# Kernel optimization log

Hardware: AMD Instinct MI355X
Metric: run time of the kernel (lower is better)

Reference implementation:

```python
import jax, jax.numpy as jnp
import numpy as np

B, T, D, K = 16, 4096, 512, 128
ALPHA_MIN = 1e-06
OMEGA_MAX = float(np.pi)
SN_EPS = 1e-06


def setup_inputs() -> dict:
    key = jax.random.key(0)
    ks = jax.random.split(key, 7)
    x = jax.random.normal(ks[0], (B, T, D), jnp.float32)
    # irregular positive step sizes, mean ~ 1/T like the uniform-grid default
    dt = jax.random.uniform(ks[1], (B, T), jnp.float32, minval=0.1, maxval=1.9) * (1.0 / T)
    # replicate reset_parameters: target_alpha ~ U(0.01, 0.2), raw = log(expm1(alpha - alpha_min))
    target_alpha = jax.random.uniform(ks[2], (K,), jnp.float32, minval=0.01, maxval=0.2)
    s_real_raw = jnp.log(jnp.expm1(jnp.maximum(target_alpha - ALPHA_MIN, 1e-08)))
    s_imag = jax.random.uniform(ks[3], (K,), jnp.float32, minval=-np.pi, maxval=np.pi)
    # kaiming-uniform-ish proj weight [K, D] and bias [K]
    W = jax.random.normal(ks[4], (K, D), jnp.float32) * (1.0 / np.sqrt(D))
    bound = 1.0 / np.sqrt(D)
    bias = jax.random.uniform(ks[5], (K,), jnp.float32, minval=-bound, maxval=bound)
    b_log = jnp.zeros((K,), jnp.float32)  # torch stores [1,1,K]; broadcasting is identical
    u_sn = jax.random.normal(ks[6], (K,), jnp.float32)  # spectral-norm power-iteration vector
    return {"x": x, "dt": dt, "s_real_raw": s_real_raw, "s_imag": s_imag,
            "W": W, "bias": bias, "b_log": b_log, "u_sn": u_sn}


def _spectral_normalize(W, u):
    # one power iteration, u/v detached (as torch.nn.utils.spectral_norm does)
    v = W.T @ u
    v = v / (jnp.linalg.norm(v) + SN_EPS)
    u2 = W @ v
    u2 = u2 / (jnp.linalg.norm(u2) + SN_EPS)
    u2 = jax.lax.stop_gradient(u2)
    v = jax.lax.stop_gradient(v)
    sigma = u2 @ (W @ v)
    return W / sigma


def reference(x, dt, s_real_raw, s_imag, W, bias, b_log, u_sn):
    # x: [B,T,D], dt: [B,T] -> lap_feats [B,T,2K]
    alpha = jax.nn.softplus(s_real_raw) + ALPHA_MIN          # [K] strictly positive decay
    omega = jnp.clip(s_imag, -OMEGA_MAX, OMEGA_MAX)          # [K]
    Wsn = _spectral_normalize(W, u_sn)
    u = jnp.einsum('btd,kd->btk', x, Wsn) + bias             # spectral-norm projection
    dt3 = dt[..., None]                                      # [B,T,1]
    rho = jnp.exp(-alpha * dt3)                              # [B,T,K]
    theta = omega * dt3
    cos_t, sin_t = jnp.cos(theta), jnp.sin(theta)
    b_gain = jnp.exp(b_log)                                  # [K]
    inj = (1.0 - rho) * (b_gain * u)                         # [B,T,K]

    def step(carry, inp):
        c, s = carry
        r, ct, st, it = inp
        c_new = r * (c * ct - s * st) + it
        s_new = r * (c * st + s * ct) + it
        return (c_new, s_new), (c_new, s_new)

    seq = (jnp.moveaxis(rho, 1, 0), jnp.moveaxis(cos_t, 1, 0),
           jnp.moveaxis(sin_t, 1, 0), jnp.moveaxis(inj, 1, 0))  # each [T,B,K]
    init = (jnp.zeros((x.shape[0], K), x.dtype), jnp.zeros((x.shape[0], K), x.dtype))
    _, (C, S) = jax.lax.scan(step, init, seq)
    C = jnp.moveaxis(C, 0, 1)  # [B,T,K]
    S = jnp.moveaxis(S, 0, 1)
    return jnp.concatenate([C, S], axis=-1)
```

## Files before the change

kernel.cpp:

```cpp
#include <hip/hip_runtime.h>
#include <stdint.h>

#define BB 16
#define TT 4096
#define DDIM 512
#define KK 128
#define TCB 128
#define NCB (TT / TCB)
#define PI_F 3.14159265358979323846f

typedef unsigned short u16;
typedef __attribute__((ext_vector_type(8))) short short8;
typedef __attribute__((ext_vector_type(4))) float f32x4;

__device__ __forceinline__ uint32_t cvt_bf16_rn(float f) {
  uint32_t u = __float_as_uint(f);
  return (u + 0x7FFFu + ((u >> 16) & 1u)) >> 16;
}
__device__ __forceinline__ uint32_t pack2(float a, float b) {
  return cvt_bf16_rn(a) | (cvt_bf16_rn(b) << 16);
}
__device__ __forceinline__ uint4 pack8(const float4 f0, const float4 f1) {
  uint4 r;
  r.x = pack2(f0.x, f0.y);
  r.y = pack2(f0.z, f0.w);
  r.z = pack2(f1.x, f1.y);
  r.w = pack2(f1.z, f1.w);
  return r;
}
__device__ __forceinline__ void gload_lds16(const void* g, void* l) {
  __builtin_amdgcn_global_load_lds(
      (const __attribute__((address_space(1))) void*)g,
      (__attribute__((address_space(3))) void*)l, 16, 0, 0);
}

__global__ __launch_bounds__(256) void k_prep(
    const float* __restrict__ W, const float* __restrict__ u_sn,
    const float* __restrict__ s_real_raw, const float* __restrict__ s_imag,
    const float* __restrict__ bias, const float* __restrict__ b_log,
    const float* __restrict__ dt,
    float* __restrict__ params, u16* __restrict__ Wp, float* __restrict__ ct) {
  int gb = blockIdx.x;
  int tid = threadIdx.x;
  if (gb < 64) {
    int idx = gb * 256 + tid;
    int k = idx >> 7;
    int d = (idx & 127) * 4;
    float4 v = *(const float4*)&W[(size_t)k * DDIM + d];
    int tile = d >> 6, dl = d & 63;
    int slot = (dl >> 3) ^ (k & 7);
    int e = dl & 7;
    size_t base = (size_t)tile * 8192 + k * 64 + slot * 8 + e;
    uint2 p;
    p.x = pack2(v.x, v.y);
    p.y = pack2(v.z, v.w);
    *(uint2*)&Wp[base] = p;
  } else if (gb < 80) {
    __shared__ float sc[256];
    int b = gb - 64;
    const float* row = dt + (size_t)b * TT;
    float* orow = ct + (size_t)b * TT;
    float loc[16];
    float s = 0.f;
    int base = tid * 16;
    for (int i = 0; i < 16; ++i) { s += row[base + i]; loc[i] = s; }
    sc[tid] = s;
    __syncthreads();
    for (int off = 1; off < 256; off <<= 1) {
      float v = (tid >= off) ? sc[tid - off] : 0.f;
      __syncthreads();
      sc[tid] += v;
      __syncthreads();
    }
    float excl = sc[tid] - s;
    for (int i = 0; i < 16; ++i) orow[base + i] = excl + loc[i];
  } else {
    __shared__ float su[KK];
    __shared__ float sv[DDIM];
    __shared__ float red[4];
    __shared__ float wred[256];
    __shared__ float s_sig;
    if (tid < KK) su[tid] = u_sn[tid];
    __syncthreads();
    for (int rep = 0; rep < 2; ++rep) {
      int d = tid + rep * 256;
      float acc = 0.f;
      for (int k = 0; k < KK; ++k) acc += W[k * DDIM + d] * su[k];
      sv[d] = acc;
    }
    __syncthreads();
    float nn = 0.f;
    for (int rep = 0; rep < 2; ++rep) { float v = sv[tid + rep * 256]; nn += v * v; }
    for (int off = 32; off > 0; off >>= 1) nn += __shfl_down(nn, off, 64);
    if ((tid & 63) == 0) red[tid >> 6] = nn;
    __syncthreads();
    float vn2 = red[0] + red[1] + red[2] + red[3];
    __syncthreads();
    float vinv = 1.f / (sqrtf(vn2) + 1e-6f);
    for (int rep = 0; rep < 2; ++rep) sv[tid + rep * 256] *= vinv;
    __syncthreads();
    {
      int k = tid & 127, q = tid >> 7;
      const float* wrow = W + (size_t)k * DDIM + q * 256;
      float p = 0.f;
      for (int d = 0; d < 256; ++d) p += wrow[d] * sv[q * 256 + d];
      wred[tid] = p;
    }
    __syncthreads();
    float wv = 0.f;
    if (tid < KK) wv = wred[tid] + wred[tid + 128];
    float q = wv * wv;
    for (int off = 32; off > 0; off >>= 1) q += __shfl_down(q, off, 64);
    if ((tid & 63) == 0) red[tid >> 6] = q;
    __syncthreads();
    if (tid == 0) {
      float wn2 = red[0] + red[1] + red[2] + red[3];
      s_sig = wn2 / (sqrtf(wn2) + 1e-6f);
    }
    __syncthreads();
    if (tid < KK) {
      float inv_sigma = 1.f / s_sig;
      float sr = s_real_raw[tid];
      float alpha = ((sr > 20.f) ? sr : log1pf(expf(sr))) + 1e-6f;
      float om = fminf(fmaxf(s_imag[tid], -PI_F), PI_F);
      float bg = expf(b_log[tid]);
      params[tid] = alpha;
      params[KK + tid] = om;
      params[2 * KK + tid] = bg * inv_sigma;
      params[3 * KK + tid] = bg * bias[tid];
    }
  }
}

__global__ __launch_bounds__(512, 4) void k_gemm(
    const float* __restrict__ x, const u16* __restrict__ Wp,
    const float* __restrict__ dt, const float* __restrict__ ct,
    const float* __restrict__ params, u16* __restrict__ itvb,
    float* __restrict__ csum_re, float* __restrict__ csum_im) {
  __shared__ __align__(16) u16 smem[32768];

  const int chunk = blockIdx.x, b = blockIdx.y;
  const int tid = threadIdx.x;
  const int wv = tid >> 6, l = tid & 63;
  const int lm = l & 15, lg = l >> 4;
  const int kw = wv & 1, tw = wv >> 1;
  const int t0 = chunk * TCB;

  const int xr = tid >> 2, xq = (tid & 3) * 16;
  const size_t xbase = ((size_t)b * TT + t0 + xr) * DDIM + xq;
  const int xs0 = ((xq >> 3) ^ (xr & 7)) * 8;
  const int xs1 = (((xq >> 3) + 1) ^ (xr & 7)) * 8;

  f32x4 acc[2][4];
#pragma unroll
  for (int m = 0; m < 2; ++m)
#pragma unroll
    for (int n = 0; n < 4; ++n) acc[m][n] = (f32x4)(0.0f);

  {
    const char* wsg = (const char*)Wp + (size_t)tid * 16;
    char* wd = (char*)smem + 32768 + tid * 16;
    gload_lds16(wsg, wd);
    gload_lds16(wsg + 8192, wd + 8192);
    const float* xp = x + xbase;
    float4 f0 = *(const float4*)(xp + 0);
    float4 f1 = *(const float4*)(xp + 4);
    float4 f2 = *(const float4*)(xp + 8);
    float4 f3 = *(const float4*)(xp + 12);
    *(uint4*)&smem[xr * 64 + xs0] = pack8(f0, f1);
    *(uint4*)&smem[xr * 64 + xs1] = pack8(f2, f3);
  }
  __syncthreads();

  int cur = 0;
  for (int it = 0; it < 8; ++it) {
    float4 f0, f1, f2, f3;
    if (it < 7) {
      const float* xp = x + xbase + (it + 1) * 64;
      f0 = *(const float4*)(xp + 0);
      f1 = *(const float4*)(xp + 4);
      f2 = *(const float4*)(xp + 8);
      f3 = *(const float4*)(xp + 12);
      const char* wsg = (const char*)Wp + (size_t)(it + 1) * 16384 + tid * 16;
      char* wd = (char*)smem + 32768 + (cur ^ 1) * 16384 + tid * 16;
      gload_lds16(wsg, wd);
      gload_lds16(wsg + 8192, wd + 8192);
    }
    __builtin_amdgcn_sched_barrier(0);
    {
      const u16* xb = smem + cur * 8192;
      const u16* wb = smem + 16384 + cur * 8192;
#pragma unroll
      for (int ks = 0; ks < 2; ++ks) {
        short8 fa[2], fb[4];
#pragma unroll
        for (int m = 0; m < 2; ++m) {
          int row = tw * 32 + m * 16 + lm;
          int sw = ((ks * 4 + lg) ^ (row & 7)) * 8;
          fa[m] = *(const short8*)&xb[row * 64 + sw];
        }
#pragma unroll
        for (int n = 0; n < 4; ++n) {
          int row = kw * 64 + n * 16 + lm;
          int sw = ((ks * 4 + lg) ^ (row & 7)) * 8;
          fb[n] = *(const short8*)&wb[row * 64 + sw];
        }
#pragma unroll
        for (int m = 0; m < 2; ++m)
#pragma unroll
          for (int n = 0; n < 4; ++n)
            acc[m][n] = __builtin_amdgcn_mfma_f32_16x16x32_bf16(fa[m], fb[n], acc[m][n], 0, 0, 0);
      }
    }
    __builtin_amdgcn_sched_barrier(0);
    if (it < 7) {
      u16* xb = smem + (cur ^ 1) * 8192;
      *(uint4*)&xb[xr * 64 + xs0] = pack8(f0, f1);
      *(uint4*)&xb[xr * 64 + xs1] = pack8(f2, f3);
    }
    __syncthreads();
    cur ^= 1;
  }

  float* totr = (float*)smem;
  float* toti = (float*)smem + 512;
  u16* litv = smem + 8192;

  float dtv[2][4], ctv[2][4];
#pragma unroll
  for (int m = 0; m < 2; ++m)
#pragma unroll
    for (int r = 0; r < 4; ++r) {
      int t = t0 + tw * 32 + m * 16 + lg * 4 + r;
      dtv[m][r] = dt[(size_t)b * TT + t];
      ctv[m][r] = ct[(size_t)b * TT + t];
    }

#pragma unroll
  for (int n = 0; n < 4; ++n) {
    int k = kw * 64 + n * 16 + lm;
    float pal = params[k], pom = params[KK + k];
    float pc1 = params[2 * KK + k], pc2 = params[3 * KK + k];
    float sr = 0.f, si2 = 0.f;
#pragma unroll
    for (int m = 0; m < 2; ++m)
#pragma unroll
      for (int r = 0; r < 4; ++r) {
        float g = acc[m][n][r];
        float a = pal * dtv[m][r];
        float omr = a * (1.f - a * (0.5f - a * (1.f / 6.f)));
        float itv = omr * (pc1 * g + pc2);
        int tl = tw * 32 + m * 16 + lg * 4 + r;
        litv[tl * KK + k] = (u16)cvt_bf16_rn(itv);
        float e = __expf(pal * ctv[m][r]);
        float sn, cs;
        __sincosf(pom * ctv[m][r], &sn, &cs);
        sr += itv * e * cs;
        si2 -= itv * e * sn;
      }
    sr += __shfl_xor(sr, 16, 64);
    sr += __shfl_xor(sr, 32, 64);
    si2 += __shfl_xor(si2, 16, 64);
    si2 += __shfl_xor(si2, 32, 64);
    if (lg == 0) { totr[tw * KK + k] = sr; toti[tw * KK + k] = si2; }
  }
  __syncthreads();

  if (tid < 256) {
    int v = tid & 127;
    float* src = (tid < 128) ? totr : toti;
    float* dst = (tid < 128) ? csum_re : csum_im;
    dst[((size_t)b * NCB + chunk) * KK + v] =
        (src[v] + src[KK + v]) + (src[2 * KK + v] + src[3 * KK + v]);
  }
  {
    int row = tid >> 4;
    int c8 = (tid & 15) * 8;
#pragma unroll
    for (int rr = 0; rr < 4; ++rr) {
      int tr = rr * 32 + row;
      uint4 v = *(const uint4*)&litv[tr * KK + c8];
      *(uint4*)&itvb[((size_t)b * TT + t0 + tr) * KK + c8] = v;
    }
  }
}

__global__ __launch_bounds__(512) void k_final(
    const u16* __restrict__ itvb, const float* __restrict__ ct,
    const float* __restrict__ params,
    const float* __restrict__ csum_re, const float* __restrict__ csum_im,
    float* __restrict__ out) {
  __shared__ float prer[KK], prei[KK];
  __shared__ float segr[16][KK], segi[16][KK];
  const int chunk = blockIdx.x, b = blockIdx.y;
  const int tid = threadIdx.x;
  const int k4 = (tid & 31) * 4, tseg = tid >> 5;
  const int tbase = chunk * TCB + tseg * 8;

  if (tid < 256) {
    int v = tid & 127;
    const float* srcp = (tid < 128) ? csum_re : csum_im;
    float* dstp = (tid < 128) ? prer : prei;
    size_t base = (size_t)b * NCB * KK + v;
    float a0 = 0.f, a1 = 0.f, a2 = 0.f, a3 = 0.f;
    int c = 0;
    for (; c + 4 <= chunk; c += 4) {
      a0 += srcp[base + (size_t)(c + 0) * KK];
      a1 += srcp[base + (size_t)(c + 1) * KK];
      a2 += srcp[base + (size_t)(c + 2) * KK];
      a3 += srcp[base + (size_t)(c + 3) * KK];
    }
    for (; c < chunk; ++c) a0 += srcp[base + (size_t)c * KK];
    dstp[v] = (a0 + a1) + (a2 + a3);
  }

  float4 pal4 = *(const float4*)&params[k4];
  float4 pom4 = *(const float4*)&params[KK + k4];
  float pal[4] = {pal4.x, pal4.y, pal4.z, pal4.w};
  float pom[4] = {pom4.x, pom4.y, pom4.z, pom4.w};

  uint2 iv8[8];
  float fr[8][4], fi[8][4];
  float sr[4] = {0.f, 0.f, 0.f, 0.f}, si[4] = {0.f, 0.f, 0.f, 0.f};
#pragma unroll
  for (int i = 0; i < 8; ++i) {
    int t = tbase + i;
    float ctv = ct[(size_t)b * TT + t];
    iv8[i] = *(const uint2*)&itvb[((size_t)b * TT + t) * KK + k4];
    float it[4] = {__uint_as_float(iv8[i].x << 16), __uint_as_float(iv8[i].x & 0xFFFF0000u),
                   __uint_as_float(iv8[i].y << 16), __uint_as_float(iv8[i].y & 0xFFFF0000u)};
#pragma unroll
    for (int c = 0; c < 4; ++c) {
      float e = __expf(pal[c] * ctv);
      float sn, cs;
      __sincosf(pom[c] * ctv, &sn, &cs);
      fr[i][c] = e * cs;
      fi[i][c] = e * sn;
      sr[c] += it[c] * fr[i][c];
      si[c] -= it[c] * fi[i][c];
    }
  }
  *(float4*)&segr[tseg][k4] = make_float4(sr[0], sr[1], sr[2], sr[3]);
  *(float4*)&segi[tseg][k4] = make_float4(si[0], si[1], si[2], si[3]);
  __syncthreads();
  float cr[4], ci[4];
  {
    float4 p0 = *(const float4*)&prer[k4];
    float4 p1 = *(const float4*)&prei[k4];
    cr[0] = p0.x; cr[1] = p0.y; cr[2] = p0.z; cr[3] = p0.w;
    ci[0] = p1.x; ci[1] = p1.y; ci[2] = p1.z; ci[3] = p1.w;
  }
  for (int s = 0; s < tseg; ++s) {
    float4 a = *(const float4*)&segr[s][k4];
    float4 bb = *(const float4*)&segi[s][k4];
    cr[0] += a.x; cr[1] += a.y; cr[2] += a.z; cr[3] += a.w;
    ci[0] += bb.x; ci[1] += bb.y; ci[2] += bb.z; ci[3] += bb.w;
  }
#pragma unroll
  for (int i = 0; i < 8; ++i) {
    int t = tbase + i;
    float it[4] = {__uint_as_float(iv8[i].x << 16), __uint_as_float(iv8[i].x & 0xFFFF0000u),
                   __uint_as_float(iv8[i].y << 16), __uint_as_float(iv8[i].y & 0xFFFF0000u)};
    float C4[4], S4[4];
#pragma unroll
    for (int c = 0; c < 4; ++c) {
      float f_r = fr[i][c], f_i = fi[i][c];
      cr[c] += it[c] * f_r;
      ci[c] -= it[c] * f_i;
      float inv = __builtin_amdgcn_rcpf(f_r * f_r + f_i * f_i);
      float Rw = (cr[c] * f_r - ci[c] * f_i) * inv;
      float Iw = (cr[c] * f_i + ci[c] * f_r) * inv;
      C4[c] = Rw - Iw;
      S4[c] = Rw + Iw;
    }
    size_t rowb = ((size_t)b * TT + t) * (2 * KK);
    *(float4*)&out[rowb + k4] = make_float4(C4[0], C4[1], C4[2], C4[3]);
    *(float4*)&out[rowb + KK + k4] = make_float4(S4[0], S4[1], S4[2], S4[3]);
  }
}

extern "C" void kernel_launch(void* const* d_in, const int* in_sizes, int n_in,
                              void* d_out, int out_size, void* d_ws, size_t ws_size,
                              hipStream_t stream) {
  const float* x    = (const float*)d_in[0];
  const float* dt   = (const float*)d_in[1];
  const float* srr  = (const float*)d_in[2];
  const float* si   = (const float*)d_in[3];
  const float* W    = (const float*)d_in[4];
  const float* bias = (const float*)d_in[5];
  const float* blog = (const float*)d_in[6];
  const float* usn  = (const float*)d_in[7];
  float* out = (float*)d_out;
  float* ws = (float*)d_ws;

  float* params  = ws;
  float* ct      = ws + 4 * KK;
  float* csum_re = ct + (size_t)BB * TT;
  float* csum_im = csum_re + (size_t)BB * NCB * KK;
  u16*   Wp      = (u16*)(csum_im + (size_t)BB * NCB * KK);
  u16*   itvb    = Wp + 65536;

  k_prep<<<81, 256, 0, stream>>>(W, usn, srr, si, bias, blog, dt, params, Wp, ct);
  k_gemm<<<dim3(NCB, BB), 512, 0, stream>>>(x, Wp, dt, ct, params, itvb,
                                            csum_re, csum_im);
  k_final<<<dim3(NCB, BB), 512, 0, stream>>>(itvb, ct, params,
                                             csum_re, csum_im, out);
}
```

Before: 67.52 us.

## Load GEMM operands directly from global into MFMA registers, drop LDS staging

The weight matrix is now prepacked in MFMA fragment order, so each lane loads its B fragment with one 16-byte global load. The x rows are read straight from global memory into registers and converted to bf16 in place. This removes the LDS double-buffer, the swizzled stores and the per-iteration barriers, and shrinks shared memory so more blocks can be resident. In exchange, x loads become strided per lane, W fragments are reread from L2 by every block, and there is less explicit prefetching.

```diff
diff --git a/kernel.cpp b/kernel.cpp
--- a/kernel.cpp
+++ b/kernel.cpp
@@ -20,18 +20,13 @@
 __device__ __forceinline__ uint32_t pack2(float a, float b) {
   return cvt_bf16_rn(a) | (cvt_bf16_rn(b) << 16);
 }
-__device__ __forceinline__ uint4 pack8(const float4 f0, const float4 f1) {
-  uint4 r;
-  r.x = pack2(f0.x, f0.y);
-  r.y = pack2(f0.z, f0.w);
-  r.z = pack2(f1.x, f1.y);
-  r.w = pack2(f1.z, f1.w);
-  return r;
-}
-__device__ __forceinline__ void gload_lds16(const void* g, void* l) {
-  __builtin_amdgcn_global_load_lds(
-      (const __attribute__((address_space(1))) void*)g,
-      (__attribute__((address_space(3))) void*)l, 16, 0, 0);
+__device__ __forceinline__ short8 pack8s(float4 f0, float4 f1) {
+  uint4 u;
+  u.x = pack2(f0.x, f0.y);
+  u.y = pack2(f0.z, f0.w);
+  u.z = pack2(f1.x, f1.y);
+  u.w = pack2(f1.z, f1.w);
+  return __builtin_bit_cast(short8, u);
 }
 
 __global__ __launch_bounds__(256) void k_prep(
@@ -39,22 +34,25 @@
     const float* __restrict__ s_real_raw, const float* __restrict__ s_imag,
     const float* __restrict__ bias, const float* __restrict__ b_log,
     const float* __restrict__ dt,
-    float* __restrict__ params, u16* __restrict__ Wp, float* __restrict__ ct) {
+    float* __restrict__ params, u16* __restrict__ Wp2, float* __restrict__ ct) {
   int gb = blockIdx.x;
   int tid = threadIdx.x;
   if (gb < 64) {
     int idx = gb * 256 + tid;
-    int k = idx >> 7;
-    int d = (idx & 127) * 4;
+    int o = idx * 4;
+    int lent = o >> 3;
+    int half = (o >> 2) & 1;
+    int ks = lent >> 9;
+    int rem = lent & 511;
+    int kg = rem >> 6;
+    int l = rem & 63;
+    int k = kg * 16 + (l & 15);
+    int d = ks * 32 + (l >> 4) * 8 + half * 4;
     float4 v = *(const float4*)&W[(size_t)k * DDIM + d];
-    int tile = d >> 6, dl = d & 63;
-    int slot = (dl >> 3) ^ (k & 7);
-    int e = dl & 7;
-    size_t base = (size_t)tile * 8192 + k * 64 + slot * 8 + e;
     uint2 p;
     p.x = pack2(v.x, v.y);
     p.y = pack2(v.z, v.w);
-    *(uint2*)&Wp[base] = p;
+    *(uint2*)&Wp2[o] = p;
   } else if (gb < 80) {
     __shared__ float sc[256];
     int b = gb - 64;
@@ -133,11 +131,11 @@
 }
 
 __global__ __launch_bounds__(512, 4) void k_gemm(
-    const float* __restrict__ x, const u16* __restrict__ Wp,
+    const float* __restrict__ x, const u16* __restrict__ Wp2,
     const float* __restrict__ dt, const float* __restrict__ ct,
     const float* __restrict__ params, u16* __restrict__ itvb,
     float* __restrict__ csum_re, float* __restrict__ csum_im) {
-  __shared__ __align__(16) u16 smem[32768];
+  __shared__ __align__(16) u16 smem[18432];
 
   const int chunk = blockIdx.x, b = blockIdx.y;
   const int tid = threadIdx.x;
@@ -146,10 +144,9 @@
   const int kw = wv & 1, tw = wv >> 1;
   const int t0 = chunk * TCB;
 
-  const int xr = tid >> 2, xq = (tid & 3) * 16;
-  const size_t xbase = ((size_t)b * TT + t0 + xr) * DDIM + xq;
-  const int xs0 = ((xq >> 3) ^ (xr & 7)) * 8;
-  const int xs1 = (((xq >> 3) + 1) ^ (xr & 7)) * 8;
+  const float* xA0 = x + ((size_t)b * TT + t0 + tw * 32 + lm) * DDIM + lg * 8;
+  const float* xA1 = xA0 + (size_t)16 * DDIM;
+  const u16* wB = Wp2 + (size_t)(kw * 4) * 512 + l * 8;
 
   f32x4 acc[2][4];
 #pragma unroll
@@ -157,74 +154,29 @@
 #pragma unroll
     for (int n = 0; n < 4; ++n) acc[m][n] = (f32x4)(0.0f);
 
-  {
-    const char* wsg = (const char*)Wp + (size_t)tid * 16;
-    char* wd = (char*)smem + 32768 + tid * 16;
-    gload_lds16(wsg, wd);
-    gload_lds16(wsg + 8192, wd + 8192);
-    const float* xp = x + xbase;
-    float4 f0 = *(const float4*)(xp + 0);
-    float4 f1 = *(const float4*)(xp + 4);
-    float4 f2 = *(const float4*)(xp + 8);
-    float4 f3 = *(const float4*)(xp + 12);
-    *(uint4*)&smem[xr * 64 + xs0] = pack8(f0, f1);
-    *(uint4*)&smem[xr * 64 + xs1] = pack8(f2, f3);
-  }
-  __syncthreads();
-
-  int cur = 0;
-  for (int it = 0; it < 8; ++it) {
-    float4 f0, f1, f2, f3;
-    if (it < 7) {
-      const float* xp = x + xbase + (it + 1) * 64;
-      f0 = *(const float4*)(xp + 0);
-      f1 = *(const float4*)(xp + 4);
-      f2 = *(const float4*)(xp + 8);
-      f3 = *(const float4*)(xp + 12);
-      const char* wsg = (const char*)Wp + (size_t)(it + 1) * 16384 + tid * 16;
-      char* wd = (char*)smem + 32768 + (cur ^ 1) * 16384 + tid * 16;
-      gload_lds16(wsg, wd);
-      gload_lds16(wsg + 8192, wd + 8192);
-    }
-    __builtin_amdgcn_sched_barrier(0);
-    {
-      const u16* xb = smem + cur * 8192;
-      const u16* wb = smem + 16384 + cur * 8192;
-#pragma unroll
-      for (int ks = 0; ks < 2; ++ks) {
-        short8 fa[2], fb[4];
-#pragma unroll
-        for (int m = 0; m < 2; ++m) {
-          int row = tw * 32 + m * 16 + lm;
-          int sw = ((ks * 4 + lg) ^ (row & 7)) * 8;
-          fa[m] = *(const short8*)&xb[row * 64 + sw];
-        }
-#pragma unroll
-        for (int n = 0; n < 4; ++n) {
-          int row = kw * 64 + n * 16 + lm;
-          int sw = ((ks * 4 + lg) ^ (row & 7)) * 8;
-          fb[n] = *(const short8*)&wb[row * 64 + sw];
-        }
-#pragma unroll
-        for (int m = 0; m < 2; ++m)
-#pragma unroll
-          for (int n = 0; n < 4; ++n)
-            acc[m][n] = __builtin_amdgcn_mfma_f32_16x16x32_bf16(fa[m], fb[n], acc[m][n], 0, 0, 0);
-      }
-    }
-    __builtin_amdgcn_sched_barrier(0);
-    if (it < 7) {
-      u16* xb = smem + (cur ^ 1) * 8192;
-      *(uint4*)&xb[xr * 64 + xs0] = pack8(f0, f1);
-      *(uint4*)&xb[xr * 64 + xs1] = pack8(f2, f3);
-    }
-    __syncthreads();
-    cur ^= 1;
-  }
-
-  float* totr = (float*)smem;
-  float* toti = (float*)smem + 512;
-  u16* litv = smem + 8192;
+#pragma unroll 4
+  for (int ks = 0; ks < 16; ++ks) {
+    float4 a00 = *(const float4*)(xA0 + ks * 32);
+    float4 a01 = *(const float4*)(xA0 + ks * 32 + 4);
+    float4 a10 = *(const float4*)(xA1 + ks * 32);
+    float4 a11 = *(const float4*)(xA1 + ks * 32 + 4);
+    short8 fb[4];
+#pragma unroll
+    for (int n = 0; n < 4; ++n)
+      fb[n] = *(const short8*)(wB + (size_t)(ks * 8 + n) * 512);
+    short8 fa[2];
+    fa[0] = pack8s(a00, a01);
+    fa[1] = pack8s(a10, a11);
+#pragma unroll
+    for (int m = 0; m < 2; ++m)
+#pragma unroll
+      for (int n = 0; n < 4; ++n)
+        acc[m][n] = __builtin_amdgcn_mfma_f32_16x16x32_bf16(fa[m], fb[n], acc[m][n], 0, 0, 0);
+  }
+
+  u16* litv = smem;
+  float* totr = (float*)(smem + 16384);
+  float* toti = totr + 512;
 
   float dtv[2][4], ctv[2][4];
 #pragma unroll
@@ -397,11 +349,11 @@
   float* ct      = ws + 4 * KK;
   float* csum_re = ct + (size_t)BB * TT;
   float* csum_im = csum_re + (size_t)BB * NCB * KK;
-  u16*   Wp      = (u16*)(csum_im + (size_t)BB * NCB * KK);
-  u16*   itvb    = Wp + 65536;
-
-  k_prep<<<81, 256, 0, stream>>>(W, usn, srr, si, bias, blog, dt, params, Wp, ct);
-  k_gemm<<<dim3(NCB, BB), 512, 0, stream>>>(x, Wp, dt, ct, params, itvb,
+  u16*   Wp2     = (u16*)(csum_im + (size_t)BB * NCB * KK);
+  u16*   itvb    = Wp2 + 65536;
+
+  k_prep<<<81, 256, 0, stream>>>(W, usn, srr, si, bias, blog, dt, params, Wp2, ct);
+  k_gemm<<<dim3(NCB, BB), 512, 0, stream>>>(x, Wp2, dt, ct, params, itvb,
                                             csum_re, csum_im);
   k_final<<<dim3(NCB, BB), 512, 0, stream>>>(itvb, ct, params,
                                              csum_re, csum_im, out);
```

Measured after the change: 82.67 us. 1.22x slower.
